# Optimization experiments

Measured on AMD Instinct MI355X. Metric: run time of the kernel, lower is better.

The kernel has to match this reference:

```python
import jax, jax.numpy as jnp
import numpy as np
import math

D_K = 64
ROUNDS = 4
BUCKET_LEN = 64


def _l2norm(x, axis):
    n = jnp.sqrt(jnp.sum(x * x, axis=axis, keepdims=True))
    return x / jnp.maximum(n, 1e-12)


def _look_back(x):
    # x: (B, n_buckets, bucket_len, ...) -> (B, n_buckets, 2*bucket_len, ...)
    # each bucket is concatenated with the previous bucket (wrapping at 0)
    shift = jnp.concatenate([x[:, -1:], x[:, :-1]], axis=1)
    return jnp.concatenate([shift, x], axis=2)


def _lsh_hash(query, rand_matrix):
    # returns position-tagged hashes: bucket_id * L + position, shape (B, L, R)
    B, L, D = query.shape
    qn = _l2norm(query, -1)
    rm = _l2norm(rand_matrix, 1)  # normalize over d_k dim, as in torch code
    xR = jnp.einsum('bld,bdrn->blrn', qn, rm)
    h = jnp.argmax(jnp.concatenate([xR, -xR], axis=-1), axis=-1).astype(jnp.int32)
    return h * L + jnp.arange(L, dtype=jnp.int32)[None, :, None]


def _attend(query, value, hash_indice, original_indice, sorted_hashes):
    B, L, D = query.shape
    nb = L // BUCKET_LEN
    R = ROUNDS
    # gather queries into hash-sorted order, per round: (B, L, D, R)
    rq = jnp.take_along_axis(query[:, :, :, None], hash_indice[:, :, None, :], axis=1)
    rq = rq.reshape(B, nb, BUCKET_LEN, D, R)
    lk = _l2norm(_look_back(rq), -2)  # keys = normalized lookback queries (shared QK)
    qk = jnp.einsum('bnijk,bnljk->bnilk', rq, lk) / math.sqrt(D_K)  # (B,nb,bl,2bl,R)
    # mask cross-bucket pairs
    sh = (sorted_hashes // L).reshape(B, nb, BUCKET_LEN, R)
    qk = jnp.where(sh[..., None, :] != _look_back(sh)[..., None, :, :], -1e9, qk)
    # mask self-attention (causal=False so no causal mask)
    qi = hash_indice.reshape(B, nb, BUCKET_LEN, R).astype(jnp.int32)
    ki = _look_back(qi)
    qk = jnp.where(qi[..., None, :] == ki[..., None, :, :], -1e5, qk)
    qk = qk.reshape(B, L, 2 * BUCKET_LEN, R)
    lse = jax.scipy.special.logsumexp(qk, axis=2)  # (B, L, R)
    p = jnp.exp(qk - lse[:, :, None, :]).reshape(B, nb, BUCKET_LEN, 2 * BUCKET_LEN, R)
    # gather values into sorted order and apply lookback attention
    rv = jnp.take_along_axis(value[:, :, :, None], hash_indice[:, :, None, :], axis=1)
    rv = rv.reshape(B, nb, BUCKET_LEN, D, R)
    att = jnp.einsum('bnijl,bnjkl->bnikl', p, _look_back(rv)).reshape(B, L, D, R)
    # scatter back to original order
    att = jnp.take_along_axis(att, original_indice[:, :, None, :], axis=1)
    lse = jnp.take_along_axis(lse, original_indice, axis=1)
    # NOTE: faithful to source, softmax over dim=1 (sequence dim)
    w = jax.nn.softmax(lse, axis=1)  # (B, L, R)
    return jnp.einsum('blir,blr->bli', att, w)  # (B, L, D)


def setup_inputs() -> dict:
    key = jax.random.key(0)
    k1, k2, k3 = jax.random.split(key, 3)
    B, L, D = 16, 8192, D_K
    n_buckets = L // BUCKET_LEN
    return {
        'query': jax.random.normal(k1, (B, L, D), jnp.float32),
        'value': jax.random.normal(k2, (B, L, D), jnp.float32),
        'rand_matrix': jax.random.normal(k3, (B, D, ROUNDS, n_buckets // 2), jnp.float32),
    }


def reference(query, value, rand_matrix):
    hashes = _lsh_hash(query, rand_matrix)          # (B, L, R) int32
    hash_indice = jnp.argsort(hashes, axis=1)       # sort positions by hash
    sorted_hashes = jnp.take_along_axis(hashes, hash_indice, axis=1)
    original_indice = jnp.argsort(hash_indice, axis=1)  # inverse permutation
    return _attend(query, value, hash_indice.astype(jnp.int32),
                   original_indice.astype(jnp.int32), sorted_hashes)
```

## Files before the change

kernel.cpp:

```cpp
#include <hip/hip_runtime.h>
#include <math.h>

#define B_   16
#define L_   8192
#define D_   64
#define R_   4
#define NB_  128
#define NH_  64

__device__ __forceinline__ float dpp_xor1(float x) {
    return __int_as_float(__builtin_amdgcn_mov_dpp(__float_as_int(x), 0xB1, 0xf, 0xf, true));
}
__device__ __forceinline__ float dpp_xor2(float x) {
    return __int_as_float(__builtin_amdgcn_mov_dpp(__float_as_int(x), 0x4E, 0xf, 0xf, true));
}
__device__ __forceinline__ float quad_bcast0(float x) {
    return __int_as_float(__builtin_amdgcn_mov_dpp(__float_as_int(x), 0x00, 0xf, 0xf, true));
}
__device__ __forceinline__ float quad_bcast1(float x) {
    return __int_as_float(__builtin_amdgcn_mov_dpp(__float_as_int(x), 0x55, 0xf, 0xf, true));
}
__device__ __forceinline__ float quad_bcast2(float x) {
    return __int_as_float(__builtin_amdgcn_mov_dpp(__float_as_int(x), 0xAA, 0xf, 0xf, true));
}
__device__ __forceinline__ float quad_bcast3(float x) {
    return __int_as_float(__builtin_amdgcn_mov_dpp(__float_as_int(x), 0xFF, 0xf, 0xf, true));
}

__global__ __launch_bounds__(64) void k_rmnorm(const float* __restrict__ rm, double* __restrict__ rmn) {
    int b = blockIdx.x >> 2, r = blockIdx.x & 3;
    int n = threadIdx.x;
    float v[D_];
    double ss = 0.0;
    #pragma unroll
    for (int d = 0; d < D_; ++d) {
        float f = rm[((size_t)(b * D_ + d) * R_ + r) * NH_ + n];
        v[d] = f;
        ss += (double)f * (double)f;
    }
    double nrm = sqrt(ss); if (nrm < 1e-12) nrm = 1e-12;
    double inv = 1.0 / nrm;
    double* o = rmn + ((size_t)(b * R_ + r) * NH_ + n) * D_;
    #pragma unroll
    for (int d = 0; d < D_; ++d) o[d] = (double)v[d] * inv;
}

__global__ __launch_bounds__(256) void k_hash(const float* __restrict__ q, const double* __restrict__ rmn,
                                              float* __restrict__ rn, int* __restrict__ h) {
    __shared__ double rmd[NH_ * D_];
    __shared__ float  rms[NH_ * D_];
    int b = blockIdx.z, r = blockIdx.y;
    int l = blockIdx.x * 256 + threadIdx.x;
    const double* src = rmn + (size_t)(b * R_ + r) * NH_ * D_;
    for (int i = threadIdx.x; i < NH_ * D_; i += 256) {
        double dv = src[i];
        rmd[i] = dv;
        rms[i] = (float)dv;
    }
    const float* qp = q + ((size_t)b * L_ + l) * D_;
    float qf[D_];
    double ss = 0.0;
    #pragma unroll
    for (int d = 0; d < D_; d += 4) {
        float4 f = *(const float4*)(qp + d);
        qf[d] = f.x; qf[d+1] = f.y; qf[d+2] = f.z; qf[d+3] = f.w;
        ss += (double)f.x * f.x + (double)f.y * f.y + (double)f.z * f.z + (double)f.w * f.w;
    }
    __syncthreads();
    float best = -1.0e30f, second = -1.0e30f; int bi = 0;
    for (int n = 0; n < NH_; ++n) {
        const float* kp = &rms[n * D_];
        float a0 = 0, a1 = 0, a2 = 0, a3 = 0;
        #pragma unroll
        for (int d = 0; d < D_; d += 4) {
            a0 = fmaf(qf[d],   kp[d],   a0);
            a1 = fmaf(qf[d+1], kp[d+1], a1);
            a2 = fmaf(qf[d+2], kp[d+2], a2);
            a3 = fmaf(qf[d+3], kp[d+3], a3);
        }
        float s = (a0 + a1) + (a2 + a3);
        if (s > best)       { second = best; best = s; bi = n; }
        else if (s > second)  second = s;
        float ns = -s;
        if (ns > best)      { second = best; best = ns; bi = n + NH_; }
        else if (ns > second) second = ns;
    }
    float qn = (float)sqrt(ss);
    if (best - second < 3.0e-5f * qn + 1.0e-7f) {
        double qd[D_];
        #pragma unroll
        for (int d = 0; d < D_; ++d) qd[d] = (double)qf[d];
        double bestd = -1.0e300; bi = 0;
        for (int n = 0; n < NH_; ++n) {
            const double* kp = &rmd[n * D_];
            double a0 = 0, a1 = 0, a2 = 0, a3 = 0;
            #pragma unroll
            for (int d = 0; d < D_; d += 4) {
                a0 = fma(qd[d],   kp[d],   a0);
                a1 = fma(qd[d+1], kp[d+1], a1);
                a2 = fma(qd[d+2], kp[d+2], a2);
                a3 = fma(qd[d+3], kp[d+3], a3);
            }
            double s = (a0 + a1) + (a2 + a3);
            if (s > bestd)  { bestd = s;  bi = n; }
            if (-s > bestd) { bestd = -s; bi = n + NH_; }
        }
    }
    h[(size_t)(b * R_ + r) * L_ + l] = bi;
    if (r == 0) {
        double nrm = sqrt(ss); if (nrm < 1e-12) nrm = 1e-12;
        rn[(size_t)b * L_ + l] = (float)(1.0 / nrm);
    }
}

__global__ __launch_bounds__(64) void k_sort(const int* __restrict__ h, int* __restrict__ idx,
                                             int* __restrict__ sb, int* __restrict__ iv) {
    __shared__ unsigned int cnt[NB_ * 64];
    int br = blockIdx.x;
    const int* hh = h + (size_t)br * L_;
    int t = threadIdx.x;
    for (int i = t; i < NB_ * 64; i += 64) cnt[i] = 0;
    __syncthreads();
    int base = t * 128;
    for (int i = 0; i < 128; ++i) { int bk = hh[base + i]; cnt[bk * 64 + t]++; }
    __syncthreads();
    int fb = t * 128;
    unsigned int local = 0;
    for (int i = 0; i < 128; ++i) local += cnt[fb + i];
    unsigned int v = local;
    #pragma unroll
    for (int off = 1; off < 64; off <<= 1) {
        unsigned int u = __shfl_up(v, off);
        if (t >= off) v += u;
    }
    unsigned int run = v - local;
    for (int i = 0; i < 128; ++i) { unsigned int c0 = cnt[fb + i]; cnt[fb + i] = run; run += c0; }
    __syncthreads();
    int* oi = idx + (size_t)br * L_;
    int* ob = sb  + (size_t)br * L_;
    int* ivp = iv + (size_t)br * L_;
    for (int i = 0; i < 128; ++i) {
        int l = base + i; int bk = hh[l];
        unsigned int pos = cnt[bk * 64 + t]++;
        oi[pos] = l; ob[pos] = bk; ivp[l] = (int)pos;
    }
}

__global__ __launch_bounds__(64, 2) void k_flash(const float* __restrict__ q, const float* __restrict__ val,
                                                 const int* __restrict__ idx, const int* __restrict__ sb,
                                                 const float* __restrict__ rn, float* __restrict__ lse,
                                                 const float* __restrict__ gm, const float* __restrict__ gs,
                                                 float* __restrict__ out, float* __restrict__ contrib,
                                                 int r_fixed, int omode) {
    __shared__ float kt[16 * 80];
    __shared__ float vt[16 * 80];
    __shared__ int   kqs[16];
    __shared__ int   kbs[16];
    __shared__ float krs[16];
    int c = blockIdx.x, b = blockIdx.z;
    int r = (r_fixed < 0) ? (int)blockIdx.y : r_fixed;
    size_t sbase = (size_t)(b * R_ + r) * L_;
    int tid = threadIdx.x;
    int h = tid & 3;
    int posq = c * 64 + (tid >> 2) * 4;
    int mls[4];
    #pragma unroll
    for (int qq = 0; qq < 4; ++qq) mls[qq] = idx[sbase + posq + qq];
    int ownpos  = posq + h;
    int myl_own = idx[sbase + ownpos];
    int mybk_own = sb[sbase + ownpos];
    float m_own = 0.125f / rn[(size_t)b * L_ + myl_own];
    const float* qb = q   + (size_t)b * L_ * D_;
    const float* vb = val + (size_t)b * L_ * D_;
    float qv[4][16];
    #pragma unroll
    for (int qq = 0; qq < 4; ++qq) {
        const float* qp = qb + (size_t)mls[qq] * D_ + h * 16;
        #pragma unroll
        for (int i = 0; i < 16; i += 4) {
            float4 f = *(const float4*)(qp + i);
            qv[qq][i] = f.x; qv[qq][i+1] = f.y; qv[qq][i+2] = f.z; qv[qq][i+3] = f.w;
        }
    }
    float ps[4] = {0.0f, 0.0f, 0.0f, 0.0f};
    float acc[4][16];
    #pragma unroll
    for (int qq = 0; qq < 4; ++qq)
        #pragma unroll
        for (int i = 0; i < 16; ++i) acc[qq][i] = 0.0f;

    #pragma unroll 1
    for (int s = 0; s < 8; ++s) {
        int ck = ((c + NB_ - 1 + (s >> 2)) & (NB_ - 1)) * 64 + (s & 3) * 16;
        __syncthreads();
        {
            int rw = tid >> 2, cc = tid & 3;
            int kl = idx[sbase + ck + rw];
            const float* kp = qb + (size_t)kl * D_ + cc * 16;
            float* kd = &kt[rw * 80 + cc * 20];
            #pragma unroll
            for (int i = 0; i < 16; i += 4) *(float4*)(kd + i) = *(const float4*)(kp + i);
            if (omode != 2) {
                const float* vp = vb + (size_t)kl * D_ + cc * 16;
                float* vd = &vt[rw * 80 + cc * 20];
                #pragma unroll
                for (int i = 0; i < 16; i += 4) *(float4*)(vd + i) = *(const float4*)(vp + i);
            }
            if (tid < 16) {
                int kl2 = idx[sbase + ck + tid];
                kqs[tid] = kl2;
                kbs[tid] = sb[sbase + ck + tid];
                krs[tid] = rn[(size_t)b * L_ + kl2] * 0.125f;
            }
        }
        __syncthreads();
        #pragma unroll
        for (int j = 0; j < 16; ++j) {
            const float* kpj = &kt[j * 80 + h * 20];
            float p0 = 0, p1 = 0, p2 = 0, p3 = 0;
            #pragma unroll
            for (int i = 0; i < 16; i += 4) {
                float4 kk = *(const float4*)(kpj + i);
                p0 = fmaf(qv[0][i], kk.x, p0); p0 = fmaf(qv[0][i+1], kk.y, p0);
                p0 = fmaf(qv[0][i+2], kk.z, p0); p0 = fmaf(qv[0][i+3], kk.w, p0);
                p1 = fmaf(qv[1][i], kk.x, p1); p1 = fmaf(qv[1][i+1], kk.y, p1);
                p1 = fmaf(qv[1][i+2], kk.z, p1); p1 = fmaf(qv[1][i+3], kk.w, p1);
                p2 = fmaf(qv[2][i], kk.x, p2); p2 = fmaf(qv[2][i+1], kk.y, p2);
                p2 = fmaf(qv[2][i+2], kk.z, p2); p2 = fmaf(qv[2][i+3], kk.w, p2);
                p3 = fmaf(qv[3][i], kk.x, p3); p3 = fmaf(qv[3][i+1], kk.y, p3);
                p3 = fmaf(qv[3][i+2], kk.z, p3); p3 = fmaf(qv[3][i+3], kk.w, p3);
            }
            bool b0 = (h & 1), b1 = (h & 2) != 0;
            float u0 = b0 ? p1 : p0;
            float t0 = b0 ? p0 : p1;
            u0 += dpp_xor1(t0);
            float u2 = b0 ? p3 : p2;
            float t2 = b0 ? p2 : p3;
            u2 += dpp_xor1(t2);
            float dot = b1 ? u2 : u0;
            float t3 = b1 ? u0 : u2;
            dot += dpp_xor2(t3);
            float sc = dot * krs[j];
            sc = (kbs[j] == mybk_own) ? sc : -1.0e9f;
            if (kqs[j] == myl_own) sc = -1.0e5f;
            float p = __expf(sc - m_own);
            ps[j & 3] += p;
            if (omode != 2) {
                float pq0 = quad_bcast0(p), pq1 = quad_bcast1(p);
                float pq2 = quad_bcast2(p), pq3 = quad_bcast3(p);
                const float* vpj = &vt[j * 80 + h * 20];
                #pragma unroll
                for (int i = 0; i < 16; i += 4) {
                    float4 vv = *(const float4*)(vpj + i);
                    acc[0][i]   = fmaf(pq0, vv.x, acc[0][i]);   acc[0][i+1] = fmaf(pq0, vv.y, acc[0][i+1]);
                    acc[0][i+2] = fmaf(pq0, vv.z, acc[0][i+2]); acc[0][i+3] = fmaf(pq0, vv.w, acc[0][i+3]);
                    acc[1][i]   = fmaf(pq1, vv.x, acc[1][i]);   acc[1][i+1] = fmaf(pq1, vv.y, acc[1][i+1]);
                    acc[1][i+2] = fmaf(pq1, vv.z, acc[1][i+2]); acc[1][i+3] = fmaf(pq1, vv.w, acc[1][i+3]);
                    acc[2][i]   = fmaf(pq2, vv.x, acc[2][i]);   acc[2][i+1] = fmaf(pq2, vv.y, acc[2][i+1]);
                    acc[2][i+2] = fmaf(pq2, vv.z, acc[2][i+2]); acc[2][i+3] = fmaf(pq2, vv.w, acc[2][i+3]);
                    acc[3][i]   = fmaf(pq3, vv.x, acc[3][i]);   acc[3][i+1] = fmaf(pq3, vv.y, acc[3][i+1]);
                    acc[3][i+2] = fmaf(pq3, vv.z, acc[3][i+2]); acc[3][i+3] = fmaf(pq3, vv.w, acc[3][i+3]);
                }
            }
        }
    }
    float sum = (ps[0] + ps[1]) + (ps[2] + ps[3]);
    float lse_own, inv_own;
    if (sum > 0.0f) { lse_own = m_own + logf(sum); inv_own = 1.0f / sum; }
    else            { lse_own = -3.0e38f;          inv_own = 0.0f; }
    if (omode != 3) lse[sbase + ownpos] = lse_own;
    if (omode == 0 || omode == 1) {
        float ivs[4];
        ivs[0] = quad_bcast0(inv_own); ivs[1] = quad_bcast1(inv_own);
        ivs[2] = quad_bcast2(inv_own); ivs[3] = quad_bcast3(inv_own);
        float* cbase = contrib + ((omode == 0) ? (size_t)(b * R_ + r) * L_ : (size_t)b * L_) * D_;
        #pragma unroll
        for (int qq = 0; qq < 4; ++qq) {
            float* cp = cbase + (size_t)(posq + qq) * D_ + h * 16;
            #pragma unroll
            for (int i = 0; i < 16; i += 4) {
                float4 o;
                o.x = acc[qq][i] * ivs[qq];   o.y = acc[qq][i+1] * ivs[qq];
                o.z = acc[qq][i+2] * ivs[qq]; o.w = acc[qq][i+3] * ivs[qq];
                *(float4*)(cp + i) = o;
            }
        }
    } else if (omode == 3) {
        int brr = b * R_ + r;
        float gmv = gm[brr], gsv = gs[brr];
        float ls4[4], iv4[4];
        ls4[0] = quad_bcast0(lse_own); ls4[1] = quad_bcast1(lse_own);
        ls4[2] = quad_bcast2(lse_own); ls4[3] = quad_bcast3(lse_own);
        iv4[0] = quad_bcast0(inv_own); iv4[1] = quad_bcast1(inv_own);
        iv4[2] = quad_bcast2(inv_own); iv4[3] = quad_bcast3(inv_own);
        #pragma unroll
        for (int qq = 0; qq < 4; ++qq) {
            float w = __expf(ls4[qq] - gmv) * gsv * iv4[qq];
            float* op = out + ((size_t)b * L_ + mls[qq]) * D_ + h * 16;
            #pragma unroll
            for (int i = 0; i < 16; ++i) unsafeAtomicAdd(op + i, w * acc[qq][i]);
        }
    }
}

__global__ __launch_bounds__(256) void k_wred(const float* __restrict__ lse, float* __restrict__ gm,
                                              float* __restrict__ gs, int r_w) {
    __shared__ float  sm[4];
    __shared__ double sd[4];
    int br = (r_w < 0) ? (int)blockIdx.x : ((int)blockIdx.x * R_ + r_w);
    const float* x = lse + (size_t)br * L_;
    int t = threadIdx.x;
    float mx = -3.0e38f;
    for (int i = t; i < L_; i += 256) mx = fmaxf(mx, x[i]);
    #pragma unroll
    for (int o = 32; o; o >>= 1) mx = fmaxf(mx, __shfl_down(mx, o));
    if ((t & 63) == 0) sm[t >> 6] = mx;
    __syncthreads();
    mx = fmaxf(fmaxf(sm[0], sm[1]), fmaxf(sm[2], sm[3]));
    double s = 0.0;
    for (int i = t; i < L_; i += 256) s += exp((double)x[i] - (double)mx);
    #pragma unroll
    for (int o = 32; o; o >>= 1) s += __shfl_down(s, o);
    if ((t & 63) == 0) sd[t >> 6] = s;
    __syncthreads();
    if (t == 0) { gm[br] = mx; gs[br] = (float)(1.0 / (sd[0] + sd[1] + sd[2] + sd[3])); }
}

__global__ __launch_bounds__(256) void k_comb_full(const float* __restrict__ contrib,
                                                   const int* __restrict__ iv,
                                                   const float* __restrict__ lse,
                                                   const float* __restrict__ gm,
                                                   const float* __restrict__ gs,
                                                   float* __restrict__ out) {
    int gid = blockIdx.x * 256 + threadIdx.x;
    int row = gid >> 2;
    int ch  = (gid & 3) * 16;
    int b = row >> 13, l = row & (L_ - 1);
    float s[16];
    #pragma unroll
    for (int i = 0; i < 16; ++i) s[i] = 0.0f;
    #pragma unroll
    for (int r = 0; r < R_; ++r) {
        int brr = b * R_ + r;
        int pos = iv[(size_t)brr * L_ + l];
        float w = expf(lse[(size_t)brr * L_ + pos] - gm[brr]) * gs[brr];
        const float* cp = contrib + ((size_t)brr * L_ + pos) * D_ + ch;
        #pragma unroll
        for (int i = 0; i < 16; i += 4) {
            float4 f = *(const float4*)(cp + i);
            s[i]   = fmaf(w, f.x, s[i]);   s[i+1] = fmaf(w, f.y, s[i+1]);
            s[i+2] = fmaf(w, f.z, s[i+2]); s[i+3] = fmaf(w, f.w, s[i+3]);
        }
    }
    float* op = out + (size_t)row * D_ + ch;
    #pragma unroll
    for (int i = 0; i < 16; i += 4) {
        float4 o; o.x = s[i]; o.y = s[i+1]; o.z = s[i+2]; o.w = s[i+3];
        *(float4*)(op + i) = o;
    }
}

__global__ __launch_bounds__(256) void k_comb_add(const float* __restrict__ contrib,
                                                  const int* __restrict__ iv,
                                                  const float* __restrict__ lse,
                                                  const float* __restrict__ gm,
                                                  const float* __restrict__ gs,
                                                  float* __restrict__ out, int r) {
    int gid = blockIdx.x * 256 + threadIdx.x;
    int row = gid >> 2;
    int ch  = (gid & 3) * 16;
    int b = row >> 13, l = row & (L_ - 1);
    int brr = b * R_ + r;
    int pos = iv[(size_t)brr * L_ + l];
    float w = expf(lse[(size_t)brr * L_ + pos] - gm[brr]) * gs[brr];
    const float* cp = contrib + ((size_t)b * L_ + pos) * D_ + ch;
    float* op = out + (size_t)row * D_ + ch;
    #pragma unroll
    for (int i = 0; i < 16; i += 4) {
        float4 f = *(const float4*)(cp + i);
        float4 o = *(const float4*)(op + i);
        o.x = fmaf(w, f.x, o.x); o.y = fmaf(w, f.y, o.y);
        o.z = fmaf(w, f.z, o.z); o.w = fmaf(w, f.w, o.w);
        *(float4*)(op + i) = o;
    }
}

#define OFF_RMN     0u
#define OFF_RN      2097152u
#define OFF_H       2621440u
#define OFF_IDX     4718592u
#define OFF_SB      6815744u
#define OFF_LSE     8912896u
#define OFF_GM      11010048u
#define OFF_GS      11010304u
#define OFF_INV     11010560u
#define OFF_CONTRIB 13107712u
#define CONTRIB_FULL_BYTES  134217728ull
#define CONTRIB_SLICE_BYTES 33554432ull

extern "C" void kernel_launch(void* const* d_in, const int* in_sizes, int n_in,
                              void* d_out, int out_size, void* d_ws, size_t ws_size,
                              hipStream_t stream) {
    const float* q  = (const float*)d_in[0];
    const float* v  = (const float*)d_in[1];
    const float* rm = (const float*)d_in[2];
    float* out = (float*)d_out;
    char* ws = (char*)d_ws;
    double* rmn = (double*)(ws + OFF_RMN);
    float*  rn  = (float*)(ws + OFF_RN);
    int*    h   = (int*)(ws + OFF_H);
    int*    idx = (int*)(ws + OFF_IDX);
    int*    sb  = (int*)(ws + OFF_SB);
    float*  lse = (float*)(ws + OFF_LSE);
    float*  gm  = (float*)(ws + OFF_GM);
    float*  gs  = (float*)(ws + OFF_GS);
    int*    iv  = (int*)(ws + OFF_INV);
    float*  contrib = (float*)(ws + OFF_CONTRIB);

    int tierA = (ws_size >= (size_t)OFF_CONTRIB + CONTRIB_FULL_BYTES) ? 1 : 0;
    int tierB = (!tierA && ws_size >= (size_t)OFF_CONTRIB + CONTRIB_SLICE_BYTES) ? 1 : 0;

    hipLaunchKernelGGL(k_rmnorm, dim3(B_ * R_), dim3(64), 0, stream, rm, rmn);
    hipLaunchKernelGGL(k_hash, dim3(L_ / 256, R_, B_), dim3(256), 0, stream, q, rmn, rn, h);
    hipLaunchKernelGGL(k_sort, dim3(B_ * R_), dim3(64), 0, stream, h, idx, sb, iv);

    if (tierA) {
        hipLaunchKernelGGL(k_flash, dim3(NB_, R_, B_), dim3(64), 0, stream, q, v, idx, sb, rn,
                           lse, gm, gs, out, contrib, -1, 0);
        hipLaunchKernelGGL(k_wred, dim3(B_ * R_), dim3(256), 0, stream, lse, gm, gs, -1);
        hipLaunchKernelGGL(k_comb_full, dim3(B_ * L_ * 4 / 256), dim3(256), 0, stream,
                           contrib, iv, lse, gm, gs, out);
    } else if (tierB) {
        hipMemsetAsync(d_out, 0, (size_t)B_ * L_ * D_ * sizeof(float), stream);
        for (int r = 0; r < R_; ++r) {
            hipLaunchKernelGGL(k_flash, dim3(NB_, 1, B_), dim3(64), 0, stream, q, v, idx, sb, rn,
                               lse, gm, gs, out, contrib, r, 1);
            hipLaunchKernelGGL(k_wred, dim3(B_), dim3(256), 0, stream, lse, gm, gs, r);
            hipLaunchKernelGGL(k_comb_add, dim3(B_ * L_ * 4 / 256), dim3(256), 0, stream,
                               contrib, iv, lse, gm, gs, out, r);
        }
    } else {
        hipMemsetAsync(d_out, 0, (size_t)B_ * L_ * D_ * sizeof(float), stream);
        hipLaunchKernelGGL(k_flash, dim3(NB_, R_, B_), dim3(64), 0, stream, q, v, idx, sb, rn,
                           lse, gm, gs, out, contrib, -1, 2);
        hipLaunchKernelGGL(k_wred, dim3(B_ * R_), dim3(256), 0, stream, lse, gm, gs, -1);
        hipLaunchKernelGGL(k_flash, dim3(NB_, R_, B_), dim3(64), 0, stream, q, v, idx, sb, rn,
                           lse, gm, gs, out, contrib, -1, 3);
    }
}
```

Measured before the change: 617.5 us.

## Pack four bucket wavefronts per block, use packed float2 FMAs, tighten hash fallback

The flash kernel now runs four independent 64-thread wavefronts per 256-thread block, each with its own shared-memory tile. The block barriers are dropped, on the assumption that each wavefront only reads tile data it wrote itself. The QK and PV inner loops are rewritten with two-wide float vectors so the compiler can emit packed FMA instructions. The hash kernel's near-tie threshold that triggers the double-precision recompute is also tightened, so fewer queries take the slow path. Risks: removing __syncthreads relies on implicit in-wave ordering of LDS accesses, the narrower threshold could flip argmax ties, and the new launch bound may cap registers.

```diff
diff --git a/kernel.cpp b/kernel.cpp
--- a/kernel.cpp
+++ b/kernel.cpp
@@ -7,6 +7,8 @@
 #define R_   4
 #define NB_  128
 #define NH_  64
+
+typedef float v2f __attribute__((ext_vector_type(2)));
 
 __device__ __forceinline__ float dpp_xor1(float x) {
     return __int_as_float(__builtin_amdgcn_mov_dpp(__float_as_int(x), 0xB1, 0xf, 0xf, true));
@@ -86,7 +88,7 @@
         else if (ns > second) second = ns;
     }
     float qn = (float)sqrt(ss);
-    if (best - second < 3.0e-5f * qn + 1.0e-7f) {
+    if (best - second < 1.2e-5f * qn + 1.0e-7f) {
         double qd[D_];
         #pragma unroll
         for (int d = 0; d < D_; ++d) qd[d] = (double)qf[d];
@@ -146,21 +148,22 @@
     }
 }
 
-__global__ __launch_bounds__(64, 2) void k_flash(const float* __restrict__ q, const float* __restrict__ val,
-                                                 const int* __restrict__ idx, const int* __restrict__ sb,
-                                                 const float* __restrict__ rn, float* __restrict__ lse,
-                                                 const float* __restrict__ gm, const float* __restrict__ gs,
-                                                 float* __restrict__ out, float* __restrict__ contrib,
-                                                 int r_fixed, int omode) {
-    __shared__ float kt[16 * 80];
-    __shared__ float vt[16 * 80];
-    __shared__ int   kqs[16];
-    __shared__ int   kbs[16];
-    __shared__ float krs[16];
-    int c = blockIdx.x, b = blockIdx.z;
+__global__ __launch_bounds__(256, 3) void k_flash(const float* __restrict__ q, const float* __restrict__ val,
+                                                  const int* __restrict__ idx, const int* __restrict__ sb,
+                                                  const float* __restrict__ rn, float* __restrict__ lse,
+                                                  const float* __restrict__ gm, const float* __restrict__ gs,
+                                                  float* __restrict__ out, float* __restrict__ contrib,
+                                                  int r_fixed, int omode) {
+    __shared__ float kt[4][16 * 80];
+    __shared__ float vt[4][16 * 80];
+    __shared__ int   kqs[4][16];
+    __shared__ int   kbs[4][16];
+    __shared__ float krs[4][16];
+    int w   = threadIdx.x >> 6;
+    int tid = threadIdx.x & 63;
+    int c = blockIdx.x * 4 + w, b = blockIdx.z;
     int r = (r_fixed < 0) ? (int)blockIdx.y : r_fixed;
     size_t sbase = (size_t)(b * R_ + r) * L_;
-    int tid = threadIdx.x;
     int h = tid & 3;
     int posq = c * 64 + (tid >> 2) * 4;
     int mls[4];
@@ -172,64 +175,66 @@
     float m_own = 0.125f / rn[(size_t)b * L_ + myl_own];
     const float* qb = q   + (size_t)b * L_ * D_;
     const float* vb = val + (size_t)b * L_ * D_;
-    float qv[4][16];
+    v2f qv2[4][8];
     #pragma unroll
     for (int qq = 0; qq < 4; ++qq) {
         const float* qp = qb + (size_t)mls[qq] * D_ + h * 16;
         #pragma unroll
         for (int i = 0; i < 16; i += 4) {
             float4 f = *(const float4*)(qp + i);
-            qv[qq][i] = f.x; qv[qq][i+1] = f.y; qv[qq][i+2] = f.z; qv[qq][i+3] = f.w;
+            qv2[qq][i >> 1]       = (v2f){f.x, f.y};
+            qv2[qq][(i >> 1) + 1] = (v2f){f.z, f.w};
         }
     }
     float ps[4] = {0.0f, 0.0f, 0.0f, 0.0f};
-    float acc[4][16];
+    v2f acc2[4][8];
     #pragma unroll
     for (int qq = 0; qq < 4; ++qq)
         #pragma unroll
-        for (int i = 0; i < 16; ++i) acc[qq][i] = 0.0f;
+        for (int i = 0; i < 8; ++i) acc2[qq][i] = (v2f){0.0f, 0.0f};
 
     #pragma unroll 1
     for (int s = 0; s < 8; ++s) {
         int ck = ((c + NB_ - 1 + (s >> 2)) & (NB_ - 1)) * 64 + (s & 3) * 16;
-        __syncthreads();
         {
             int rw = tid >> 2, cc = tid & 3;
             int kl = idx[sbase + ck + rw];
             const float* kp = qb + (size_t)kl * D_ + cc * 16;
-            float* kd = &kt[rw * 80 + cc * 20];
+            float* kd = &kt[w][rw * 80 + cc * 20];
             #pragma unroll
             for (int i = 0; i < 16; i += 4) *(float4*)(kd + i) = *(const float4*)(kp + i);
             if (omode != 2) {
                 const float* vp = vb + (size_t)kl * D_ + cc * 16;
-                float* vd = &vt[rw * 80 + cc * 20];
+                float* vd = &vt[w][rw * 80 + cc * 20];
                 #pragma unroll
                 for (int i = 0; i < 16; i += 4) *(float4*)(vd + i) = *(const float4*)(vp + i);
             }
             if (tid < 16) {
                 int kl2 = idx[sbase + ck + tid];
-                kqs[tid] = kl2;
-                kbs[tid] = sb[sbase + ck + tid];
-                krs[tid] = rn[(size_t)b * L_ + kl2] * 0.125f;
-            }
-        }
-        __syncthreads();
+                kqs[w][tid] = kl2;
+                kbs[w][tid] = sb[sbase + ck + tid];
+                krs[w][tid] = rn[(size_t)b * L_ + kl2] * 0.125f;
+            }
+        }
         #pragma unroll
         for (int j = 0; j < 16; ++j) {
-            const float* kpj = &kt[j * 80 + h * 20];
-            float p0 = 0, p1 = 0, p2 = 0, p3 = 0;
+            const float* kpj = &kt[w][j * 80 + h * 20];
+            v2f a0 = (v2f){0.f, 0.f}, a1 = a0, a2 = a0, a3 = a0;
             #pragma unroll
             for (int i = 0; i < 16; i += 4) {
                 float4 kk = *(const float4*)(kpj + i);
-                p0 = fmaf(qv[0][i], kk.x, p0); p0 = fmaf(qv[0][i+1], kk.y, p0);
-                p0 = fmaf(qv[0][i+2], kk.z, p0); p0 = fmaf(qv[0][i+3], kk.w, p0);
-                p1 = fmaf(qv[1][i], kk.x, p1); p1 = fmaf(qv[1][i+1], kk.y, p1);
-                p1 = fmaf(qv[1][i+2], kk.z, p1); p1 = fmaf(qv[1][i+3], kk.w, p1);
-                p2 = fmaf(qv[2][i], kk.x, p2); p2 = fmaf(qv[2][i+1], kk.y, p2);
-                p2 = fmaf(qv[2][i+2], kk.z, p2); p2 = fmaf(qv[2][i+3], kk.w, p2);
-                p3 = fmaf(qv[3][i], kk.x, p3); p3 = fmaf(qv[3][i+1], kk.y, p3);
-                p3 = fmaf(qv[3][i+2], kk.z, p3); p3 = fmaf(qv[3][i+3], kk.w, p3);
-            }
+                v2f kA = (v2f){kk.x, kk.y}, kB = (v2f){kk.z, kk.w};
+                int i2 = i >> 1;
+                a0 = __builtin_elementwise_fma(qv2[0][i2], kA, a0);
+                a0 = __builtin_elementwise_fma(qv2[0][i2 + 1], kB, a0);
+                a1 = __builtin_elementwise_fma(qv2[1][i2], kA, a1);
+                a1 = __builtin_elementwise_fma(qv2[1][i2 + 1], kB, a1);
+                a2 = __builtin_elementwise_fma(qv2[2][i2], kA, a2);
+                a2 = __builtin_elementwise_fma(qv2[2][i2 + 1], kB, a2);
+                a3 = __builtin_elementwise_fma(qv2[3][i2], kA, a3);
+                a3 = __builtin_elementwise_fma(qv2[3][i2 + 1], kB, a3);
+            }
+            float p0 = a0.x + a0.y, p1 = a1.x + a1.y, p2 = a2.x + a2.y, p3 = a3.x + a3.y;
             bool b0 = (h & 1), b1 = (h & 2) != 0;
             float u0 = b0 ? p1 : p0;
             float t0 = b0 ? p0 : p1;
@@ -240,26 +245,30 @@
             float dot = b1 ? u2 : u0;
             float t3 = b1 ? u0 : u2;
             dot += dpp_xor2(t3);
-            float sc = dot * krs[j];
-            sc = (kbs[j] == mybk_own) ? sc : -1.0e9f;
-            if (kqs[j] == myl_own) sc = -1.0e5f;
+            float sc = dot * krs[w][j];
+            sc = (kbs[w][j] == mybk_own) ? sc : -1.0e9f;
+            if (kqs[w][j] == myl_own) sc = -1.0e5f;
             float p = __expf(sc - m_own);
             ps[j & 3] += p;
             if (omode != 2) {
-                float pq0 = quad_bcast0(p), pq1 = quad_bcast1(p);
-                float pq2 = quad_bcast2(p), pq3 = quad_bcast3(p);
-                const float* vpj = &vt[j * 80 + h * 20];
+                v2f P0 = (v2f){quad_bcast0(p), quad_bcast0(p)};
+                v2f P1 = (v2f){quad_bcast1(p), quad_bcast1(p)};
+                v2f P2 = (v2f){quad_bcast2(p), quad_bcast2(p)};
+                v2f P3 = (v2f){quad_bcast3(p), quad_bcast3(p)};
+                const float* vpj = &vt[w][j * 80 + h * 20];
                 #pragma unroll
                 for (int i = 0; i < 16; i += 4) {
                     float4 vv = *(const float4*)(vpj + i);
-                    acc[0][i]   = fmaf(pq0, vv.x, acc[0][i]);   acc[0][i+1] = fmaf(pq0, vv.y, acc[0][i+1]);
-                    acc[0][i+2] = fmaf(pq0, vv.z, acc[0][i+2]); acc[0][i+3] = fmaf(pq0, vv.w, acc[0][i+3]);
-                    acc[1][i]   = fmaf(pq1, vv.x, acc[1][i]);   acc[1][i+1] = fmaf(pq1, vv.y, acc[1][i+1]);
-                    acc[1][i+2] = fmaf(pq1, vv.z, acc[1][i+2]); acc[1][i+3] = fmaf(pq1, vv.w, acc[1][i+3]);
-                    acc[2][i]   = fmaf(pq2, vv.x, acc[2][i]);   acc[2][i+1] = fmaf(pq2, vv.y, acc[2][i+1]);
-                    acc[2][i+2] = fmaf(pq2, vv.z, acc[2][i+2]); acc[2][i+3] = fmaf(pq2, vv.w, acc[2][i+3]);
-                    acc[3][i]   = fmaf(pq3, vv.x, acc[3][i]);   acc[3][i+1] = fmaf(pq3, vv.y, acc[3][i+1]);
-                    acc[3][i+2] = fmaf(pq3, vv.z, acc[3][i+2]); acc[3][i+3] = fmaf(pq3, vv.w, acc[3][i+3]);
+                    v2f vA = (v2f){vv.x, vv.y}, vB = (v2f){vv.z, vv.w};
+                    int i2 = i >> 1;
+                    acc2[0][i2]     = __builtin_elementwise_fma(P0, vA, acc2[0][i2]);
+                    acc2[0][i2 + 1] = __builtin_elementwise_fma(P0, vB, acc2[0][i2 + 1]);
+                    acc2[1][i2]     = __builtin_elementwise_fma(P1, vA, acc2[1][i2]);
+                    acc2[1][i2 + 1] = __builtin_elementwise_fma(P1, vB, acc2[1][i2 + 1]);
+                    acc2[2][i2]     = __builtin_elementwise_fma(P2, vA, acc2[2][i2]);
+                    acc2[2][i2 + 1] = __builtin_elementwise_fma(P2, vB, acc2[2][i2 + 1]);
+                    acc2[3][i2]     = __builtin_elementwise_fma(P3, vA, acc2[3][i2]);
+                    acc2[3][i2 + 1] = __builtin_elementwise_fma(P3, vB, acc2[3][i2 + 1]);
                 }
             }
         }
@@ -279,9 +288,10 @@
             float* cp = cbase + (size_t)(posq + qq) * D_ + h * 16;
             #pragma unroll
             for (int i = 0; i < 16; i += 4) {
+                int i2 = i >> 1;
                 float4 o;
-                o.x = acc[qq][i] * ivs[qq];   o.y = acc[qq][i+1] * ivs[qq];
-                o.z = acc[qq][i+2] * ivs[qq]; o.w = acc[qq][i+3] * ivs[qq];
+                o.x = acc2[qq][i2].x * ivs[qq];     o.y = acc2[qq][i2].y * ivs[qq];
+                o.z = acc2[qq][i2 + 1].x * ivs[qq]; o.w = acc2[qq][i2 + 1].y * ivs[qq];
                 *(float4*)(cp + i) = o;
             }
         }
@@ -295,10 +305,13 @@
         iv4[2] = quad_bcast2(inv_own); iv4[3] = quad_bcast3(inv_own);
         #pragma unroll
         for (int qq = 0; qq < 4; ++qq) {
-            float w = __expf(ls4[qq] - gmv) * gsv * iv4[qq];
+            float wq = __expf(ls4[qq] - gmv) * gsv * iv4[qq];
             float* op = out + ((size_t)b * L_ + mls[qq]) * D_ + h * 16;
             #pragma unroll
-            for (int i = 0; i < 16; ++i) unsafeAtomicAdd(op + i, w * acc[qq][i]);
+            for (int i = 0; i < 8; ++i) {
+                unsafeAtomicAdd(op + 2 * i,     wq * acc2[qq][i].x);
+                unsafeAtomicAdd(op + 2 * i + 1, wq * acc2[qq][i].y);
+            }
         }
     }
 }
@@ -425,7 +438,7 @@
     hipLaunchKernelGGL(k_sort, dim3(B_ * R_), dim3(64), 0, stream, h, idx, sb, iv);
 
     if (tierA) {
-        hipLaunchKernelGGL(k_flash, dim3(NB_, R_, B_), dim3(64), 0, stream, q, v, idx, sb, rn,
+        hipLaunchKernelGGL(k_flash, dim3(NB_ / 4, R_, B_), dim3(256), 0, stream, q, v, idx, sb, rn,
                            lse, gm, gs, out, contrib, -1, 0);
         hipLaunchKernelGGL(k_wred, dim3(B_ * R_), dim3(256), 0, stream, lse, gm, gs, -1);
         hipLaunchKernelGGL(k_comb_full, dim3(B_ * L_ * 4 / 256), dim3(256), 0, stream,
@@ -433,7 +446,7 @@
     } else if (tierB) {
         hipMemsetAsync(d_out, 0, (size_t)B_ * L_ * D_ * sizeof(float), stream);
         for (int r = 0; r < R_; ++r) {
-            hipLaunchKernelGGL(k_flash, dim3(NB_, 1, B_), dim3(64), 0, stream, q, v, idx, sb, rn,
+            hipLaunchKernelGGL(k_flash, dim3(NB_ / 4, 1, B_), dim3(256), 0, stream, q, v, idx, sb, rn,
                                lse, gm, gs, out, contrib, r, 1);
             hipLaunchKernelGGL(k_wred, dim3(B_), dim3(256), 0, stream, lse, gm, gs, r);
             hipLaunchKernelGGL(k_comb_add, dim3(B_ * L_ * 4 / 256), dim3(256), 0, stream,
@@ -441,10 +454,10 @@
         }
     } else {
         hipMemsetAsync(d_out, 0, (size_t)B_ * L_ * D_ * sizeof(float), stream);
-        hipLaunchKernelGGL(k_flash, dim3(NB_, R_, B_), dim3(64), 0, stream, q, v, idx, sb, rn,
+        hipLaunchKernelGGL(k_flash, dim3(NB_ / 4, R_, B_), dim3(256), 0, stream, q, v, idx, sb, rn,
                            lse, gm, gs, out, contrib, -1, 2);
         hipLaunchKernelGGL(k_wred, dim3(B_ * R_), dim3(256), 0, stream, lse, gm, gs, -1);
-        hipLaunchKernelGGL(k_flash, dim3(NB_, R_, B_), dim3(64), 0, stream, q, v, idx, sb, rn,
+        hipLaunchKernelGGL(k_flash, dim3(NB_ / 4, R_, B_), dim3(256), 0, stream, q, v, idx, sb, rn,
                            lse, gm, gs, out, contrib, -1, 3);
     }
 }
```

After: 651.8 us. +5.5%, slower.
